# Optimization experiments

Hardware: AMD Instinct MI355X
Metric: run time of the kernel (lower is better)

Reference implementation:

```python
import jax, jax.numpy as jnp
import numpy as np

B, S, D, H, E = 4, 2048, 1024, 16, 64  # batch, seq, d_model, heads, head_dim


def setup_inputs() -> dict:
    root = jax.random.key(0)
    ks = jax.random.split(root, 12)
    std = 0.02
    inp = {
        'query': jax.random.normal(ks[0], (B, S, D), jnp.float32),
        'key':   jax.random.normal(ks[1], (B, S, D), jnp.float32),
        'value': jax.random.normal(ks[2], (B, S, D), jnp.float32),
        # per-head Dense projection params, stacked over heads
        'Wq': jax.random.normal(ks[3], (H, D, E), jnp.float32) * std,
        'bq': jnp.zeros((H, E), jnp.float32),
        'Wk': jax.random.normal(ks[4], (H, D, E), jnp.float32) * std,
        'bk': jnp.zeros((H, E), jnp.float32),
        'Wv': jax.random.normal(ks[5], (H, D, E), jnp.float32) * std,
        'bv': jnp.zeros((H, E), jnp.float32),
        # output Dense back to d_model
        'Wo': jax.random.normal(ks[6], (H * E, D), jnp.float32) * std,
        'bo': jnp.zeros((D,), jnp.float32),
        # head_selector: nn.initializers.uniform() -> U[0, 0.01)
        'head_selector': jax.random.uniform(ks[7], (H,), jnp.float32) * 0.01,
    }
    return inp


def reference(query, key, value, Wq, bq, Wk, bk, Wv, bv, Wo, bo, head_selector):
    head_weights = jax.nn.softmax(head_selector)  # [H]
    # per-head projections (vectorized over heads)
    q = jnp.einsum('bsd,hde->bhse', query, Wq) + bq[None, :, None, :]
    k = jnp.einsum('btd,hde->bhte', key,   Wk) + bk[None, :, None, :]
    v = jnp.einsum('btd,hde->bhte', value, Wv) + bv[None, :, None, :]
    scale = 1.0 / jnp.sqrt(jnp.asarray(E, q.dtype))
    scores = jnp.einsum('bhse,bhte->bhst', q, k) * scale  # [B,H,S,S]
    probs = jax.nn.softmax(scores, axis=-1)
    ctx = jnp.einsum('bhst,bhte->bhse', probs, v)
    ctx = ctx * head_weights[None, :, None, None]  # learned per-head scalar
    combined = jnp.transpose(ctx, (0, 2, 1, 3)).reshape(query.shape[0], query.shape[1], H * E)
    return combined @ Wo + bo
```

## Files before the change

kernel.cpp:

```cpp
#include <hip/hip_runtime.h>


typedef __attribute__((ext_vector_type(8))) short     s16x8;
typedef __attribute__((ext_vector_type(4))) float     f32x4;
typedef __attribute__((ext_vector_type(8))) unsigned short u16x8;
typedef __attribute__((ext_vector_type(4))) unsigned short u16x4;
typedef __attribute__((ext_vector_type(4))) unsigned int   u32x4;

#define GLD16(g, l) __builtin_amdgcn_global_load_lds(                         \
    (const __attribute__((address_space(1))) void*)(g),                       \
    (__attribute__((address_space(3))) void*)(l), 16, 0, 0)

__device__ __forceinline__ unsigned short f2bf(float f) {
  unsigned u = __builtin_bit_cast(unsigned, f);
  u += 0x7fffu + ((u >> 16) & 1u);
  return (unsigned short)(u >> 16);
}

__device__ __forceinline__ f32x4 mfma16(s16x8 a, s16x8 b, f32x4 c) {
  return __builtin_amdgcn_mfma_f32_16x16x32_bf16(a, b, c, 0, 0, 0);
}


__global__ __launch_bounds__(256) void cvt_all(
    const float* __restrict__ q, const float* __restrict__ k,
    const float* __restrict__ v, unsigned short* __restrict__ xq,
    unsigned short* __restrict__ xk, unsigned short* __restrict__ xv) {
  const int z = blockIdx.y;
  const float* in = z == 0 ? q : z == 1 ? k : v;
  unsigned short* out = z == 0 ? xq : z == 1 ? xk : xv;
  const int i = blockIdx.x * 256 + threadIdx.x;
  const float4* p = (const float4*)in;
  float4 a = p[(size_t)i * 2], b = p[(size_t)i * 2 + 1];
  u16x8 r = { f2bf(a.x), f2bf(a.y), f2bf(a.z), f2bf(a.w),
              f2bf(b.x), f2bf(b.y), f2bf(b.z), f2bf(b.w) };
  *(u16x8*)(out + (size_t)i * 8) = r;
}

__global__ __launch_bounds__(256) void pack_all(
    const float* __restrict__ Wq, const float* __restrict__ Wk,
    const float* __restrict__ Wv, const float* __restrict__ Wo,
    unsigned short* __restrict__ WQT, unsigned short* __restrict__ WKT,
    unsigned short* __restrict__ WVT, unsigned short* __restrict__ WOT) {
  __shared__ float t[64][65];
  const int z = blockIdx.z, xb = blockIdx.x, kb = blockIdx.y;
  const int tid = threadIdx.x, kr = tid >> 2, q4 = tid & 3;

  const float* srcp;
  size_t srs;
  if (z < 3) {
    const float* W = z == 0 ? Wq : z == 1 ? Wk : Wv;
    srcp = W + (size_t)xb * 65536 + (size_t)kb * 4096;
    srs = 64;
  } else {
    srcp = Wo + (size_t)kb * 65536 + (size_t)xb * 64;
    srs = 1024;
  }
  unsigned short* dstb =
      (z == 0 ? WQT : z == 1 ? WKT : z == 2 ? WVT : WOT) +
      (size_t)xb * 65536 + (size_t)kb * 64;

#pragma unroll
  for (int j4 = 0; j4 < 4; ++j4) {
    float4 v = *(const float4*)(srcp + (size_t)kr * srs + q4 * 16 + j4 * 4);
    t[kr][q4 * 16 + j4 * 4 + 0] = v.x;
    t[kr][q4 * 16 + j4 * 4 + 1] = v.y;
    t[kr][q4 * 16 + j4 * 4 + 2] = v.z;
    t[kr][q4 * 16 + j4 * 4 + 3] = v.w;
  }
  __syncthreads();

  const int er = tid >> 2;
  u16x8 lo, hi;
#pragma unroll
  for (int j = 0; j < 8; ++j) lo[j] = f2bf(t[q4 * 16 + j][er]);
#pragma unroll
  for (int j = 0; j < 8; ++j) hi[j] = f2bf(t[q4 * 16 + 8 + j][er]);
  unsigned short* d = dstb + (size_t)er * 1024 + q4 * 16;
  *(u16x8*)d = lo;
  *(u16x8*)(d + 8) = hi;
}

#define STAGE_G(BUF, KT)                                                      \
  {                                                                           \
    const int k0q = (KT) * 32;                                                \
    _Pragma("unroll") for (int r = 0; r < 2; ++r) {                           \
      const int row = r * 64 + srow, sr = row >> 1;                           \
      const int sch = (((row & 1) << 2) | sslot) ^ (sr & 7);                  \
      const size_t roff =                                                     \
          (size_t)(sr * 2 + (sch >> 2)) * 2048 + k0q * 2 + (sch & 3) * 16;    \
      GLD16((const char*)A + (size_t)m0 * 2048 + roff,                        \
            (char*)sA[BUF] + r * 4096 + w * 1024);                            \
      GLD16((const char*)Bt + (size_t)n0 * 2048 + roff,                       \
            (char*)sB[BUF] + r * 4096 + w * 1024);                            \
    }                                                                         \
  }

__global__ __launch_bounds__(256, 2) void gemm_qkv(
    const unsigned short* __restrict__ Xq, const unsigned short* __restrict__ Xk,
    const unsigned short* __restrict__ Xv,
    const unsigned short* __restrict__ Wqt, const unsigned short* __restrict__ Wkt,
    const unsigned short* __restrict__ Wvt,
    const float* __restrict__ bq, const float* __restrict__ bk,
    const float* __restrict__ bv,
    unsigned short* __restrict__ Qp, unsigned short* __restrict__ Kp,
    unsigned short* __restrict__ Vt) {
  const int L = blockIdx.x;
  const int W = (L & 7) * 192 + (L >> 3);
  const int z = W >> 9, vy = (W >> 3) & 63, vx = W & 7;

  const unsigned short* A  = z == 0 ? Xq : z == 1 ? Xk : Xv;
  const unsigned short* Bt = z == 0 ? Wqt : z == 1 ? Wkt : Wvt;
  const float* bias = z == 0 ? bq : z == 1 ? bk : bv;

  __shared__ unsigned short sA[2][128 * 32], sB[2][128 * 32];
  const int tid = threadIdx.x, w = tid >> 6, l = tid & 63, g = l >> 4, c = l & 15;
  const int m0 = vy * 128, n0 = vx * 128;
  const int wrow = (w >> 1) * 64, wcol = (w & 1) * 64;
  const int srow = tid >> 2, sslot = tid & 3;

  f32x4 acc[4][4] = {};

  STAGE_G(0, 0);
  __syncthreads();

  for (int kt = 0; kt < 32; ++kt) {
    const int cur = kt & 1;
    if (kt + 1 < 32) STAGE_G(cur ^ 1, kt + 1);
    s16x8 af[4], bfr[4];
#pragma unroll
    for (int mi = 0; mi < 4; ++mi) {
      const int row = wrow + mi * 16 + c;
      const int ch = (((row & 1) << 2) | g) ^ ((row >> 1) & 7);
      af[mi] = *(const s16x8*)&sA[cur][(row >> 1) * 64 + ch * 8];
    }
#pragma unroll
    for (int ni = 0; ni < 4; ++ni) {
      const int row = wcol + ni * 16 + c;
      const int ch = (((row & 1) << 2) | g) ^ ((row >> 1) & 7);
      bfr[ni] = *(const s16x8*)&sB[cur][(row >> 1) * 64 + ch * 8];
    }
#pragma unroll
    for (int mi = 0; mi < 4; ++mi)
#pragma unroll
      for (int ni = 0; ni < 4; ++ni)
        acc[mi][ni] = mfma16(af[mi], bfr[ni], acc[mi][ni]);
    __syncthreads();
  }

#pragma unroll
  for (int ni = 0; ni < 4; ++ni) {
    const int n = n0 + wcol + ni * 16 + c;
    const float bn = bias[n];
    const int h = n >> 6, e = n & 63;
#pragma unroll
    for (int mi = 0; mi < 4; ++mi) {
      const int m = m0 + wrow + mi * 16 + 4 * g;
      const int b = m >> 11, s = m & 2047;
      if (z == 2) {
        u16x4 o;
#pragma unroll
        for (int i = 0; i < 4; ++i) o[i] = f2bf(acc[mi][ni][i] + bn);
        *(u16x4*)&Vt[(((size_t)(b * 16 + h) * 64 + e) << 11) + s] = o;
      } else {
        unsigned short* dst = (z == 0) ? Qp : Kp;
        const float scale = (z == 0) ? 0.1803368801111244f : 1.0f;
        const size_t base = (((size_t)(b * 16 + h) << 11) + s) << 6;
#pragma unroll
        for (int i = 0; i < 4; ++i)
          dst[base + (size_t)i * 64 + e] = f2bf((acc[mi][ni][i] + bn) * scale);
      }
    }
  }
}

__global__ __launch_bounds__(256, 4) void attn(
    const unsigned short* __restrict__ Qp, const unsigned short* __restrict__ Kp,
    const unsigned short* __restrict__ Vt, const float* __restrict__ hsel,
    unsigned short* __restrict__ Cmb) {
  __shared__ char smem[16384];

  const int tid = threadIdx.x, w = tid >> 6, l = tid & 63, g = l >> 4, c = l & 15;
  const int L  = blockIdx.x;
  const int Lp = (L & 7) * 128 + (L >> 3);
  const int bh = Lp >> 4, qb = Lp & 15;
  const int b = bh >> 4, h = bh & 15;

  float hm = -1e30f, hs = 0.f;
  for (int i = 0; i < 16; ++i) hm = fmaxf(hm, hsel[i]);
  for (int i = 0; i < 16; ++i) hs += __expf(hsel[i] - hm);
  const float hw = __expf(hsel[h] - hm) / hs;

  const size_t qbase = ((size_t)bh * 2048 + qb * 128 + w * 32) * 64;
  s16x8 qf[2][2];
#pragma unroll
  for (int nt = 0; nt < 2; ++nt)
#pragma unroll
    for (int ks = 0; ks < 2; ++ks)
      qf[nt][ks] = *(const s16x8*)(Qp + qbase + (size_t)(nt * 16 + c) * 64 +
                                   ks * 32 + 8 * g);

  f32x4 accc[4][2] = {};
  f32x4 lacc[2] = {};
  const short ob = (short)0x3F80;
  const s16x8 ones = { ob, ob, ob, ob, ob, ob, ob, ob };

  const size_t kbase = (size_t)bh * 2048 * 128;
  const size_t vbase = (size_t)bh * 64 * 4096;
  const int krow = tid >> 3, kslot = tid & 7;
  const size_t kroff = kbase + (size_t)krow * 128 + (size_t)((kslot ^ (krow & 7)) * 16);
  const int vrow = tid >> 2, vslot = tid & 3, vsr = vrow >> 1;
  const int vsch = (((vrow & 1) << 2) | vslot) ^ (vsr & 7);
  const size_t vroff = vbase + (size_t)(vsr * 2 + (vsch >> 2)) * 4096 + (vsch & 3) * 16;

  GLD16((const char*)Kp + kroff, smem + w * 1024);
  GLD16((const char*)Vt + vroff, smem + 4096 + w * 1024);
  __syncthreads();

  for (int it = 0; it < 64; ++it) {
    const int cur = it & 1;
    if (it + 1 < 64) {
      const size_t t0 = (size_t)(it + 1) * 32;
      GLD16((const char*)Kp + kroff + t0 * 128, smem + (cur ^ 1) * 8192 + w * 1024);
      GLD16((const char*)Vt + vroff + t0 * 2,   smem + (cur ^ 1) * 8192 + 4096 + w * 1024);
    }
    const unsigned short* sK = (const unsigned short*)(smem + cur * 8192);
    const unsigned short* sV = (const unsigned short*)(smem + cur * 8192 + 4096);

    f32x4 st[2][2] = {};
#pragma unroll
    for (int ks = 0; ks < 2; ++ks)
#pragma unroll
      for (int mt = 0; mt < 2; ++mt) {
        const int tr = mt * 16 + c;
        s16x8 kf = *(const s16x8*)&sK[tr * 64 + (((4 * ks + g) ^ (tr & 7)) << 3)];
#pragma unroll
        for (int nt = 0; nt < 2; ++nt)
          st[mt][nt] = mfma16(kf, qf[nt][ks], st[mt][nt]);
      }

    s16x8 pf[2];
#pragma unroll
    for (int nt = 0; nt < 2; ++nt) {
#pragma unroll
      for (int mt = 0; mt < 2; ++mt)
#pragma unroll
        for (int i = 0; i < 4; ++i)
          st[mt][nt][i] = __builtin_amdgcn_exp2f(st[mt][nt][i]);

      unsigned a0, a1, b0, b1;
      asm("v_cvt_pk_bf16_f32 %0, %1, %2" : "=v"(a0) : "v"(st[0][nt][0]), "v"(st[0][nt][1]));
      asm("v_cvt_pk_bf16_f32 %0, %1, %2" : "=v"(a1) : "v"(st[0][nt][2]), "v"(st[0][nt][3]));
      asm("v_cvt_pk_bf16_f32 %0, %1, %2" : "=v"(b0) : "v"(st[1][nt][0]), "v"(st[1][nt][1]));
      asm("v_cvt_pk_bf16_f32 %0, %1, %2" : "=v"(b1) : "v"(st[1][nt][2]), "v"(st[1][nt][3]));
      asm("v_permlane32_swap_b32 %0, %1" : "+v"(a0), "+v"(b0));
      asm("v_permlane16_swap_b32 %0, %1" : "+v"(a0), "+v"(b0));
      asm("v_permlane32_swap_b32 %0, %1" : "+v"(a1), "+v"(b1));
      asm("v_permlane16_swap_b32 %0, %1" : "+v"(a1), "+v"(b1));
      u32x4 pd = { a0, a1, b0, b1 };
      pf[nt] = __builtin_bit_cast(s16x8, pd);
      lacc[nt] = mfma16(ones, pf[nt], lacc[nt]);
    }

#pragma unroll
    for (int et = 0; et < 4; ++et) {
      const int er = et * 16 + c;
      const int ch = (((er & 1) << 2) | g) ^ ((er >> 1) & 7);
      s16x8 vf = *(const s16x8*)&sV[(er >> 1) * 64 + ch * 8];
#pragma unroll
      for (int nt = 0; nt < 2; ++nt)
        accc[et][nt] = mfma16(vf, pf[nt], accc[et][nt]);
    }
    __syncthreads();
  }

#pragma unroll
  for (int nt = 0; nt < 2; ++nt) {
    const float sc = hw / lacc[nt][0];
    const int s = qb * 128 + w * 32 + nt * 16 + c;
    unsigned short* dst = Cmb + (((size_t)(b * 2048 + s)) << 10) + h * 64;
#pragma unroll
    for (int et = 0; et < 4; ++et) {
      u16x4 o = { f2bf(accc[et][nt][0] * sc), f2bf(accc[et][nt][1] * sc),
                  f2bf(accc[et][nt][2] * sc), f2bf(accc[et][nt][3] * sc) };
      *(u16x4*)(dst + et * 16 + 4 * g) = o;
    }
  }
}

__global__ __launch_bounds__(256, 2) void gemm_out(
    const unsigned short* __restrict__ A, const unsigned short* __restrict__ Bt,
    const float* __restrict__ bo, float* __restrict__ out) {
  const int L = blockIdx.x;
  const int W = (L & 7) * 64 + (L >> 3);
  const int vy = W >> 3, vx = W & 7;

  __shared__ unsigned short sA[2][128 * 32], sB[2][128 * 32];
  const int tid = threadIdx.x, w = tid >> 6, l = tid & 63, g = l >> 4, c = l & 15;
  const int m0 = vy * 128, n0 = vx * 128;
  const int wrow = (w >> 1) * 64, wcol = (w & 1) * 64;
  const int srow = tid >> 2, sslot = tid & 3;

  f32x4 acc[4][4] = {};

  STAGE_G(0, 0);
  __syncthreads();

  for (int kt = 0; kt < 32; ++kt) {
    const int cur = kt & 1;
    if (kt + 1 < 32) STAGE_G(cur ^ 1, kt + 1);
    s16x8 af[4], bfr[4];
#pragma unroll
    for (int mi = 0; mi < 4; ++mi) {
      const int row = wrow + mi * 16 + c;
      const int ch = (((row & 1) << 2) | g) ^ ((row >> 1) & 7);
      af[mi] = *(const s16x8*)&sA[cur][(row >> 1) * 64 + ch * 8];
    }
#pragma unroll
    for (int ni = 0; ni < 4; ++ni) {
      const int row = wcol + ni * 16 + c;
      const int ch = (((row & 1) << 2) | g) ^ ((row >> 1) & 7);
      bfr[ni] = *(const s16x8*)&sB[cur][(row >> 1) * 64 + ch * 8];
    }
#pragma unroll
    for (int mi = 0; mi < 4; ++mi)
#pragma unroll
      for (int ni = 0; ni < 4; ++ni)
        acc[mi][ni] = mfma16(af[mi], bfr[ni], acc[mi][ni]);
    __syncthreads();
  }

#pragma unroll
  for (int ni = 0; ni < 4; ++ni) {
    const int n = n0 + wcol + ni * 16 + c;
    const float bn = bo[n];
#pragma unroll
    for (int mi = 0; mi < 4; ++mi) {
      const int m = m0 + wrow + mi * 16 + 4 * g;
#pragma unroll
      for (int i = 0; i < 4; ++i)
        out[(size_t)(m + i) * 1024 + n] = acc[mi][ni][i] + bn;
    }
  }
}

extern "C" void kernel_launch(void* const* d_in, const int* in_sizes, int n_in,
                              void* d_out, int out_size, void* d_ws, size_t ws_size,
                              hipStream_t stream) {
  const float* query = (const float*)d_in[0];
  const float* key   = (const float*)d_in[1];
  const float* value = (const float*)d_in[2];
  const float* Wq    = (const float*)d_in[3];
  const float* bq    = (const float*)d_in[4];
  const float* Wk    = (const float*)d_in[5];
  const float* bk    = (const float*)d_in[6];
  const float* Wv    = (const float*)d_in[7];
  const float* bv    = (const float*)d_in[8];
  const float* Wo    = (const float*)d_in[9];
  const float* bo    = (const float*)d_in[10];
  const float* hsel  = (const float*)d_in[11];
  float* out = (float*)d_out;

  char* ws = (char*)d_ws;
  const size_t SZX = 16777216;
  const size_t SZW = 2097152;
  unsigned short* XQ  = (unsigned short*)(ws);
  unsigned short* XK  = (unsigned short*)(ws + SZX);
  unsigned short* XV  = (unsigned short*)(ws + 2 * SZX);
  unsigned short* WQT = (unsigned short*)(ws + 3 * SZX);
  unsigned short* WKT = (unsigned short*)(ws + 3 * SZX + SZW);
  unsigned short* WVT = (unsigned short*)(ws + 3 * SZX + 2 * SZW);
  unsigned short* WOT = (unsigned short*)(ws + 3 * SZX + 3 * SZW);
  unsigned short* QP  = (unsigned short*)(ws + 3 * SZX + 4 * SZW);
  unsigned short* KP  = (unsigned short*)(ws + 4 * SZX + 4 * SZW);
  unsigned short* VTP = (unsigned short*)(ws + 5 * SZX + 4 * SZW);
  unsigned short* CMB = (unsigned short*)(ws + 6 * SZX + 4 * SZW);

  cvt_all<<<dim3(4096, 3), 256, 0, stream>>>(query, key, value, XQ, XK, XV);
  pack_all<<<dim3(16, 16, 4), 256, 0, stream>>>(Wq, Wk, Wv, Wo, WQT, WKT, WVT, WOT);
  gemm_qkv<<<1536, 256, 0, stream>>>(XQ, XK, XV, WQT, WKT, WVT,
                                     bq, bk, bv, QP, KP, VTP);
  attn<<<1024, 256, 0, stream>>>(QP, KP, VTP, hsel, CMB);
  gemm_out<<<512, 256, 0, stream>>>(CMB, WOT, bo, out);
}
```

Measured before the change: 340.6 us.

## Rewrite QKV projection GEMM with 256x256 tiles, 8 waves and interleaved pipeline

The QKV projection GEMM now uses 256x256 output tiles per 512-thread block with a 64-wide K step and 128 KB of double-buffered LDS. Global-to-LDS loads for the next K tile are interleaved with MFMA quarter-phases, separated by barriers and raised wave priority. The goal is more operand reuse per LDS byte and better overlap of memory traffic with matrix math. In exchange it uses a large LDS footprint, more registers and only 384 blocks, which may limit occupancy and balance across CUs.

```diff
diff --git a/kernel.cpp b/kernel.cpp
--- a/kernel.cpp
+++ b/kernel.cpp
@@ -81,22 +81,44 @@
   *(u16x8*)(d + 8) = hi;
 }
 
-#define STAGE_G(BUF, KT)                                                      \
-  {                                                                           \
-    const int k0q = (KT) * 32;                                                \
-    _Pragma("unroll") for (int r = 0; r < 2; ++r) {                           \
-      const int row = r * 64 + srow, sr = row >> 1;                           \
-      const int sch = (((row & 1) << 2) | sslot) ^ (sr & 7);                  \
-      const size_t roff =                                                     \
-          (size_t)(sr * 2 + (sch >> 2)) * 2048 + k0q * 2 + (sch & 3) * 16;    \
-      GLD16((const char*)A + (size_t)m0 * 2048 + roff,                        \
-            (char*)sA[BUF] + r * 4096 + w * 1024);                            \
-      GLD16((const char*)Bt + (size_t)n0 * 2048 + roff,                       \
-            (char*)sB[BUF] + r * 4096 + w * 1024);                            \
-    }                                                                         \
-  }
-
-__global__ __launch_bounds__(256, 2) void gemm_qkv(
+
+#define STG(gb, h, dbase, kt)                                                  \
+  GLD16((gb) + (size_t)((h) * 128 + slr) * 2048 + (kt) * 128 + sch,            \
+        smem + (dbase) + (h) * 16384 + wid * 1024);                            \
+  GLD16((gb) + (size_t)((h) * 128 + 64 + slr) * 2048 + (kt) * 128 + sch,       \
+        smem + (dbase) + (h) * 16384 + 8192 + wid * 1024);
+
+#define LDA(buf, mq)                                                           \
+  _Pragma("unroll") for (int mi = 0; mi < 4; ++mi)                             \
+  _Pragma("unroll") for (int ks = 0; ks < 2; ++ks)                             \
+    afr[mi][ks] = *(const s16x8*)(smem + (buf) * 65536 + wr * 16384 +          \
+        ((mq) * 64 + mi * 16 + c) * 128 + (((ks * 4 + g) ^ (c & 7)) << 4));
+
+#define LDB(buf, nq)                                                           \
+  _Pragma("unroll") for (int ni = 0; ni < 2; ++ni)                             \
+  _Pragma("unroll") for (int ks = 0; ks < 2; ++ks)                             \
+    bfr[(nq) * 2 + ni][ks] = *(const s16x8*)(smem + (buf) * 65536 + 32768 +    \
+        (wc >> 1) * 16384 + ((wc & 1) * 64 + ((nq) * 2 + ni) * 16 + c) * 128 + \
+        (((ks * 4 + g) ^ (c & 7)) << 4));
+
+#define MMA(mq, nq)                                                            \
+  __builtin_amdgcn_s_setprio(1);                                               \
+  _Pragma("unroll") for (int ks = 0; ks < 2; ++ks)                             \
+  _Pragma("unroll") for (int mi = 0; mi < 4; ++mi)                             \
+  _Pragma("unroll") for (int ni = 0; ni < 2; ++ni)                             \
+    acc[(mq) * 4 + mi][(nq) * 2 + ni] = mfma16(                                \
+        afr[mi][ks], bfr[(nq) * 2 + ni][ks], acc[(mq) * 4 + mi][(nq) * 2 + ni]);\
+  __builtin_amdgcn_s_setprio(0);
+
+#define BAR() __builtin_amdgcn_s_barrier()
+#define SYNCV()                                                                \
+  do {                                                                         \
+    asm volatile("s_waitcnt vmcnt(0)" ::: "memory");                           \
+    __builtin_amdgcn_s_barrier();                                              \
+    __builtin_amdgcn_sched_barrier(0);                                         \
+  } while (0)
+
+__global__ __launch_bounds__(512, 2) void gemm_qkv8(
     const unsigned short* __restrict__ Xq, const unsigned short* __restrict__ Xk,
     const unsigned short* __restrict__ Xv,
     const unsigned short* __restrict__ Wqt, const unsigned short* __restrict__ Wkt,
@@ -105,57 +127,54 @@
     const float* __restrict__ bv,
     unsigned short* __restrict__ Qp, unsigned short* __restrict__ Kp,
     unsigned short* __restrict__ Vt) {
+  __shared__ char smem[131072];
+
+  const int tid = threadIdx.x, wid = tid >> 6, lane = tid & 63;
+  const int g = lane >> 4, c = lane & 15;
+  const int wr = wid >> 2, wc = wid & 3;
+
   const int L = blockIdx.x;
-  const int W = (L & 7) * 192 + (L >> 3);
-  const int z = W >> 9, vy = (W >> 3) & 63, vx = W & 7;
+  const int W = (L & 7) * 48 + (L >> 3);
+  const int z = W >> 7, rem = W & 127, by = rem >> 2, bx = rem & 3;
+  const int m0 = by * 256, n0 = bx * 256;
 
   const unsigned short* A  = z == 0 ? Xq : z == 1 ? Xk : Xv;
   const unsigned short* Bt = z == 0 ? Wqt : z == 1 ? Wkt : Wvt;
   const float* bias = z == 0 ? bq : z == 1 ? bk : bv;
 
-  __shared__ unsigned short sA[2][128 * 32], sB[2][128 * 32];
-  const int tid = threadIdx.x, w = tid >> 6, l = tid & 63, g = l >> 4, c = l & 15;
-  const int m0 = vy * 128, n0 = vx * 128;
-  const int wrow = (w >> 1) * 64, wcol = (w & 1) * 64;
-  const int srow = tid >> 2, sslot = tid & 3;
-
-  f32x4 acc[4][4] = {};
-
-  STAGE_G(0, 0);
-  __syncthreads();
-
-  for (int kt = 0; kt < 32; ++kt) {
-    const int cur = kt & 1;
-    if (kt + 1 < 32) STAGE_G(cur ^ 1, kt + 1);
-    s16x8 af[4], bfr[4];
-#pragma unroll
-    for (int mi = 0; mi < 4; ++mi) {
-      const int row = wrow + mi * 16 + c;
-      const int ch = (((row & 1) << 2) | g) ^ ((row >> 1) & 7);
-      af[mi] = *(const s16x8*)&sA[cur][(row >> 1) * 64 + ch * 8];
-    }
-#pragma unroll
-    for (int ni = 0; ni < 4; ++ni) {
-      const int row = wcol + ni * 16 + c;
-      const int ch = (((row & 1) << 2) | g) ^ ((row >> 1) & 7);
-      bfr[ni] = *(const s16x8*)&sB[cur][(row >> 1) * 64 + ch * 8];
-    }
-#pragma unroll
-    for (int mi = 0; mi < 4; ++mi)
-#pragma unroll
-      for (int ni = 0; ni < 4; ++ni)
-        acc[mi][ni] = mfma16(af[mi], bfr[ni], acc[mi][ni]);
-    __syncthreads();
+  const char* Ab = (const char*)A  + (size_t)m0 * 2048;
+  const char* Bb = (const char*)Bt + (size_t)n0 * 2048;
+
+  const int slr = (wid << 3) + ((lane >> 3) & 7);
+  const int sch = ((lane & 7) ^ ((lane >> 3) & 7)) << 4;
+
+  f32x4 acc[8][4] = {};
+  s16x8 afr[4][2], bfr[4][2];
+
+  STG(Ab, 0, 0, 0); STG(Ab, 1, 0, 0);
+  STG(Bb, 0, 32768, 0); STG(Bb, 1, 32768, 0);
+  SYNCV();
+
+  for (int it = 0; it < 8; ++it) {
+    const int ktB = 2 * it + 1, ktN = 2 * it + 2;
+    LDA(0, 0); LDB(0, 0); STG(Ab, 0, 65536, ktB);        BAR(); MMA(0, 0); BAR();
+    LDB(0, 1);            STG(Ab, 1, 65536, ktB);        BAR(); MMA(0, 1); BAR();
+    LDA(0, 1);            STG(Bb, 0, 65536 + 32768, ktB);BAR(); MMA(1, 0); BAR();
+                          STG(Bb, 1, 65536 + 32768, ktB);BAR(); MMA(1, 1); SYNCV();
+    LDA(1, 0); LDB(1, 0); if (it < 7) { STG(Ab, 0, 0, ktN); }     BAR(); MMA(0, 0); BAR();
+    LDB(1, 1);            if (it < 7) { STG(Ab, 1, 0, ktN); }     BAR(); MMA(0, 1); BAR();
+    LDA(1, 1);            if (it < 7) { STG(Bb, 0, 32768, ktN); } BAR(); MMA(1, 0); BAR();
+                          if (it < 7) { STG(Bb, 1, 32768, ktN); } BAR(); MMA(1, 1); SYNCV();
   }
 
 #pragma unroll
   for (int ni = 0; ni < 4; ++ni) {
-    const int n = n0 + wcol + ni * 16 + c;
+    const int n = n0 + wc * 64 + ni * 16 + c;
     const float bn = bias[n];
     const int h = n >> 6, e = n & 63;
 #pragma unroll
-    for (int mi = 0; mi < 4; ++mi) {
-      const int m = m0 + wrow + mi * 16 + 4 * g;
+    for (int mi = 0; mi < 8; ++mi) {
+      const int m = m0 + wr * 128 + mi * 16 + 4 * g;
       const int b = m >> 11, s = m & 2047;
       if (z == 2) {
         u16x4 o;
@@ -288,6 +307,21 @@
   }
 }
 
+#define STAGE_G(BUF, KT)                                                      \
+  {                                                                           \
+    const int k0q = (KT) * 32;                                                \
+    _Pragma("unroll") for (int r = 0; r < 2; ++r) {                           \
+      const int row = r * 64 + srow, sr = row >> 1;                           \
+      const int sch2 = (((row & 1) << 2) | sslot) ^ (sr & 7);                 \
+      const size_t roff =                                                     \
+          (size_t)(sr * 2 + (sch2 >> 2)) * 2048 + k0q * 2 + (sch2 & 3) * 16;  \
+      GLD16((const char*)A + (size_t)m0 * 2048 + roff,                        \
+            (char*)sA[BUF] + r * 4096 + w * 1024);                            \
+      GLD16((const char*)Bt + (size_t)n0 * 2048 + roff,                       \
+            (char*)sB[BUF] + r * 4096 + w * 1024);                            \
+    }                                                                         \
+  }
+
 __global__ __launch_bounds__(256, 2) void gemm_out(
     const unsigned short* __restrict__ A, const unsigned short* __restrict__ Bt,
     const float* __restrict__ bo, float* __restrict__ out) {
@@ -309,7 +343,7 @@
   for (int kt = 0; kt < 32; ++kt) {
     const int cur = kt & 1;
     if (kt + 1 < 32) STAGE_G(cur ^ 1, kt + 1);
-    s16x8 af[4], bfr[4];
+    s16x8 af[4], bfr2[4];
 #pragma unroll
     for (int mi = 0; mi < 4; ++mi) {
       const int row = wrow + mi * 16 + c;
@@ -320,13 +354,13 @@
     for (int ni = 0; ni < 4; ++ni) {
       const int row = wcol + ni * 16 + c;
       const int ch = (((row & 1) << 2) | g) ^ ((row >> 1) & 7);
-      bfr[ni] = *(const s16x8*)&sB[cur][(row >> 1) * 64 + ch * 8];
+      bfr2[ni] = *(const s16x8*)&sB[cur][(row >> 1) * 64 + ch * 8];
     }
 #pragma unroll
     for (int mi = 0; mi < 4; ++mi)
 #pragma unroll
       for (int ni = 0; ni < 4; ++ni)
-        acc[mi][ni] = mfma16(af[mi], bfr[ni], acc[mi][ni]);
+        acc[mi][ni] = mfma16(af[mi], bfr2[ni], acc[mi][ni]);
     __syncthreads();
   }
 
@@ -378,7 +412,7 @@
 
   cvt_all<<<dim3(4096, 3), 256, 0, stream>>>(query, key, value, XQ, XK, XV);
   pack_all<<<dim3(16, 16, 4), 256, 0, stream>>>(Wq, Wk, Wv, Wo, WQT, WKT, WVT, WOT);
-  gemm_qkv<<<1536, 256, 0, stream>>>(XQ, XK, XV, WQT, WKT, WVT,
+  gemm_qkv8<<<384, 512, 0, stream>>>(XQ, XK, XV, WQT, WKT, WVT,
                                      bq, bk, bv, QP, KP, VTP);
   attn<<<1024, 256, 0, stream>>>(QP, KP, VTP, hsel, CMB);
   gemm_out<<<512, 256, 0, stream>>>(CMB, WOT, bo, out);
```

After: 344.8 us. No clear change (+1.2%).

## Rewrite QKV projection GEMM with 256x256 tiles and 4-stage LDS pipeline

Applied to the files above, without the earlier changes.

Replaces the 128x128 double-buffered QKV GEMM with a 512-thread kernel computing 256x256 tiles, using a 4-slot shared-memory ring (128KB) filled by async global-to-LDS loads with explicit vmcnt waits. The MFMA work is split into two half-phases interleaved with staging of the next A and B slices, and s_setprio raises priority during the MFMA bursts. The aim is more operand reuse per loaded byte and better overlap of loads with matrix math. In exchange it uses a very large LDS footprint, which together with 512 threads per block limits occupancy; the declared 2 blocks per CU cannot both fit in LDS. It also launches only 384 blocks, which may leave the machine underfilled.

```diff
diff --git a/kernel.cpp b/kernel.cpp
--- a/kernel.cpp
+++ b/kernel.cpp
@@ -81,22 +81,17 @@
   *(u16x8*)(d + 8) = hi;
 }
 
-#define STAGE_G(BUF, KT)                                                      \
-  {                                                                           \
-    const int k0q = (KT) * 32;                                                \
-    _Pragma("unroll") for (int r = 0; r < 2; ++r) {                           \
-      const int row = r * 64 + srow, sr = row >> 1;                           \
-      const int sch = (((row & 1) << 2) | sslot) ^ (sr & 7);                  \
-      const size_t roff =                                                     \
-          (size_t)(sr * 2 + (sch >> 2)) * 2048 + k0q * 2 + (sch & 3) * 16;    \
-      GLD16((const char*)A + (size_t)m0 * 2048 + roff,                        \
-            (char*)sA[BUF] + r * 4096 + w * 1024);                            \
-      GLD16((const char*)Bt + (size_t)n0 * 2048 + roff,                       \
-            (char*)sB[BUF] + r * 4096 + w * 1024);                            \
-    }                                                                         \
-  }
-
-__global__ __launch_bounds__(256, 2) void gemm_qkv(
+
+#define STGA2(SL3, KS64)                                                       \
+  { char* db = smem + (SL3) * 32768;                                           \
+    GLD16(Ab + srcoff0 + (KS64), db + dst0);                                   \
+    GLD16(Ab + srcoff1 + (KS64), db + dst1); }
+#define STGB2(SL3, KS64)                                                       \
+  { char* db = smem + (SL3) * 32768 + 16384;                                   \
+    GLD16(Bb + srcoff0 + (KS64), db + dst0);                                   \
+    GLD16(Bb + srcoff1 + (KS64), db + dst1); }
+
+__global__ __launch_bounds__(512, 2) void gemm_qkv8(
     const unsigned short* __restrict__ Xq, const unsigned short* __restrict__ Xk,
     const unsigned short* __restrict__ Xv,
     const unsigned short* __restrict__ Wqt, const unsigned short* __restrict__ Wkt,
@@ -105,57 +100,96 @@
     const float* __restrict__ bv,
     unsigned short* __restrict__ Qp, unsigned short* __restrict__ Kp,
     unsigned short* __restrict__ Vt) {
+  __shared__ char smem[131072];
+
+  const int tid = threadIdx.x, wid = tid >> 6, lane = tid & 63;
+  const int g = lane >> 4, c = lane & 15;
+  const int wr = wid >> 2, wc = wid & 3;
+
   const int L = blockIdx.x;
-  const int W = (L & 7) * 192 + (L >> 3);
-  const int z = W >> 9, vy = (W >> 3) & 63, vx = W & 7;
+  const int W = (L & 7) * 48 + (L >> 3);
+  const int z = W >> 7, rem = W & 127, by = rem >> 2, bx = rem & 3;
+  const int m0 = by * 256, n0 = bx * 256;
 
   const unsigned short* A  = z == 0 ? Xq : z == 1 ? Xk : Xv;
   const unsigned short* Bt = z == 0 ? Wqt : z == 1 ? Wkt : Wvt;
   const float* bias = z == 0 ? bq : z == 1 ? bk : bv;
 
-  __shared__ unsigned short sA[2][128 * 32], sB[2][128 * 32];
-  const int tid = threadIdx.x, w = tid >> 6, l = tid & 63, g = l >> 4, c = l & 15;
-  const int m0 = vy * 128, n0 = vx * 128;
-  const int wrow = (w >> 1) * 64, wcol = (w & 1) * 64;
-  const int srow = tid >> 2, sslot = tid & 3;
-
-  f32x4 acc[4][4] = {};
-
-  STAGE_G(0, 0);
-  __syncthreads();
-
-  for (int kt = 0; kt < 32; ++kt) {
-    const int cur = kt & 1;
-    if (kt + 1 < 32) STAGE_G(cur ^ 1, kt + 1);
-    s16x8 af[4], bfr[4];
-#pragma unroll
-    for (int mi = 0; mi < 4; ++mi) {
-      const int row = wrow + mi * 16 + c;
-      const int ch = (((row & 1) << 2) | g) ^ ((row >> 1) & 7);
-      af[mi] = *(const s16x8*)&sA[cur][(row >> 1) * 64 + ch * 8];
-    }
-#pragma unroll
-    for (int ni = 0; ni < 4; ++ni) {
-      const int row = wcol + ni * 16 + c;
-      const int ch = (((row & 1) << 2) | g) ^ ((row >> 1) & 7);
-      bfr[ni] = *(const s16x8*)&sB[cur][(row >> 1) * 64 + ch * 8];
-    }
+  const char* Ab = (const char*)A  + (size_t)m0 * 2048;
+  const char* Bb = (const char*)Bt + (size_t)n0 * 2048;
+
+  const int d0 = tid, sr0 = d0 >> 3, j0 = (d0 & 7) ^ (sr0 & 7);
+  const int d1 = tid + 512, sr1 = d1 >> 3, j1 = (d1 & 7) ^ (sr1 & 7);
+  const int srcoff0 = (sr0 * 2 + (j0 >> 2)) * 2048 + (j0 & 3) * 16;
+  const int srcoff1 = (sr1 * 2 + (j1 >> 2)) * 2048 + (j1 & 3) * 16;
+  const int dst0 = wid * 1024, dst1 = 8192 + wid * 1024;
+
+  int aoff[8], boff[4];
+#pragma unroll
+  for (int mi = 0; mi < 8; ++mi) {
+    const int row = wr * 128 + mi * 16 + c;
+    aoff[mi] = (row >> 1) * 128 + (((((row & 1) << 2) | g) ^ ((row >> 1) & 7)) << 4);
+  }
+#pragma unroll
+  for (int ni = 0; ni < 4; ++ni) {
+    const int row = wc * 64 + ni * 16 + c;
+    boff[ni] = 16384 + (row >> 1) * 128 +
+               (((((row & 1) << 2) | g) ^ ((row >> 1) & 7)) << 4);
+  }
+
+  f32x4 acc[8][4] = {};
+
+  STGA2(0, 0);   STGB2(0, 0);
+  STGA2(1, 64);  STGB2(1, 64);
+  STGA2(2, 128); STGB2(2, 128);
+
+  for (int s = 0; s < 32; ++s) {
+    if (s < 30)       asm volatile("s_waitcnt vmcnt(8)" ::: "memory");
+    else if (s == 30) asm volatile("s_waitcnt vmcnt(4)" ::: "memory");
+    else              asm volatile("s_waitcnt vmcnt(0)" ::: "memory");
+    __builtin_amdgcn_s_barrier();
+    __builtin_amdgcn_sched_barrier(0);
+
+    const char* sb = smem + (s & 3) * 32768;
+    const int sl3 = (s + 3) & 3, ks64 = (s + 3) * 64;
+    s16x8 afr[4], bfr[4], afr2[4];
+
+#pragma unroll
+    for (int mi = 0; mi < 4; ++mi) afr[mi] = *(const s16x8*)(sb + aoff[mi]);
+#pragma unroll
+    for (int ni = 0; ni < 4; ++ni) bfr[ni] = *(const s16x8*)(sb + boff[ni]);
+    if (s < 29) STGA2(sl3, ks64);
+    __builtin_amdgcn_s_barrier();
+    __builtin_amdgcn_s_setprio(1);
 #pragma unroll
     for (int mi = 0; mi < 4; ++mi)
 #pragma unroll
       for (int ni = 0; ni < 4; ++ni)
-        acc[mi][ni] = mfma16(af[mi], bfr[ni], acc[mi][ni]);
-    __syncthreads();
+        acc[mi][ni] = mfma16(afr[mi], bfr[ni], acc[mi][ni]);
+    __builtin_amdgcn_s_setprio(0);
+    __builtin_amdgcn_s_barrier();
+
+#pragma unroll
+    for (int mi = 0; mi < 4; ++mi) afr2[mi] = *(const s16x8*)(sb + aoff[4 + mi]);
+    if (s < 29) STGB2(sl3, ks64);
+    __builtin_amdgcn_s_barrier();
+    __builtin_amdgcn_s_setprio(1);
+#pragma unroll
+    for (int mi = 0; mi < 4; ++mi)
+#pragma unroll
+      for (int ni = 0; ni < 4; ++ni)
+        acc[4 + mi][ni] = mfma16(afr2[mi], bfr[ni], acc[4 + mi][ni]);
+    __builtin_amdgcn_s_setprio(0);
   }
 
 #pragma unroll
   for (int ni = 0; ni < 4; ++ni) {
-    const int n = n0 + wcol + ni * 16 + c;
+    const int n = n0 + wc * 64 + ni * 16 + c;
     const float bn = bias[n];
     const int h = n >> 6, e = n & 63;
 #pragma unroll
-    for (int mi = 0; mi < 4; ++mi) {
-      const int m = m0 + wrow + mi * 16 + 4 * g;
+    for (int mi = 0; mi < 8; ++mi) {
+      const int m = m0 + wr * 128 + mi * 16 + 4 * g;
       const int b = m >> 11, s = m & 2047;
       if (z == 2) {
         u16x4 o;
@@ -288,6 +322,21 @@
   }
 }
 
+#define STAGE_G(BUF, KT)                                                      \
+  {                                                                           \
+    const int k0q = (KT) * 32;                                                \
+    _Pragma("unroll") for (int r = 0; r < 2; ++r) {                           \
+      const int row = r * 64 + srow, sr = row >> 1;                           \
+      const int sch2 = (((row & 1) << 2) | sslot) ^ (sr & 7);                 \
+      const size_t roff =                                                     \
+          (size_t)(sr * 2 + (sch2 >> 2)) * 2048 + k0q * 2 + (sch2 & 3) * 16;  \
+      GLD16((const char*)A + (size_t)m0 * 2048 + roff,                        \
+            (char*)sA[BUF] + r * 4096 + w * 1024);                            \
+      GLD16((const char*)Bt + (size_t)n0 * 2048 + roff,                       \
+            (char*)sB[BUF] + r * 4096 + w * 1024);                            \
+    }                                                                         \
+  }
+
 __global__ __launch_bounds__(256, 2) void gemm_out(
     const unsigned short* __restrict__ A, const unsigned short* __restrict__ Bt,
     const float* __restrict__ bo, float* __restrict__ out) {
@@ -309,7 +358,7 @@
   for (int kt = 0; kt < 32; ++kt) {
     const int cur = kt & 1;
     if (kt + 1 < 32) STAGE_G(cur ^ 1, kt + 1);
-    s16x8 af[4], bfr[4];
+    s16x8 af[4], bfr2[4];
 #pragma unroll
     for (int mi = 0; mi < 4; ++mi) {
       const int row = wrow + mi * 16 + c;
@@ -320,13 +369,13 @@
     for (int ni = 0; ni < 4; ++ni) {
       const int row = wcol + ni * 16 + c;
       const int ch = (((row & 1) << 2) | g) ^ ((row >> 1) & 7);
-      bfr[ni] = *(const s16x8*)&sB[cur][(row >> 1) * 64 + ch * 8];
+      bfr2[ni] = *(const s16x8*)&sB[cur][(row >> 1) * 64 + ch * 8];
     }
 #pragma unroll
     for (int mi = 0; mi < 4; ++mi)
 #pragma unroll
       for (int ni = 0; ni < 4; ++ni)
-        acc[mi][ni] = mfma16(af[mi], bfr[ni], acc[mi][ni]);
+        acc[mi][ni] = mfma16(af[mi], bfr2[ni], acc[mi][ni]);
     __syncthreads();
   }
 
@@ -378,7 +427,7 @@
 
   cvt_all<<<dim3(4096, 3), 256, 0, stream>>>(query, key, value, XQ, XK, XV);
   pack_all<<<dim3(16, 16, 4), 256, 0, stream>>>(Wq, Wk, Wv, Wo, WQT, WKT, WVT, WOT);
-  gemm_qkv<<<1536, 256, 0, stream>>>(XQ, XK, XV, WQT, WKT, WVT,
+  gemm_qkv8<<<384, 512, 0, stream>>>(XQ, XK, XV, WQT, WKT, WVT,
                                      bq, bk, bv, QP, KP, VTP);
   attn<<<1024, 256, 0, stream>>>(QP, KP, VTP, hsel, CMB);
   gemm_out<<<512, 256, 0, stream>>>(CMB, WOT, bo, out);
```

Result: no change. 346.0 us (+1.6%).
